# Optimization experiments

Hardware: AMD Instinct MI355X
Metric: run time of the kernel (lower is better)

The kernel has to match this reference:

```python
import jax, jax.numpy as jnp
import numpy as np

E = 131072          # number of message events
NUM_NODES = 32768   # max distinct dst ids (unique padded to this size)
D_MEM = 256         # memory dim
D_EDGE = 128        # edge feature dim
T_DIM = 64          # time encoding dim
HID = 512           # message MLP hidden
MSG = 256           # message dim (GRU input)
IN_DIM = 2 * D_MEM + D_EDGE + T_DIM  # 704


def setup_inputs() -> dict:
    key = jax.random.key(0)
    ks = jax.random.split(key, 16)
    def lin(k, fan_out, fan_in):
        s = 1.0 / np.sqrt(fan_in)
        return jax.random.uniform(k, (fan_out, fan_in), jnp.float32, -s, s)
    def vec(k, n, fan_in):
        s = 1.0 / np.sqrt(fan_in)
        return jax.random.uniform(k, (n,), jnp.float32, -s, s)
    return {
        "rel_time": jax.random.uniform(ks[0], (E,), jnp.float32, 0.0, 1.0) * 1000.0,
        "src_memories": jax.random.normal(ks[1], (E, D_MEM), jnp.float32),
        "dst_memories": jax.random.normal(ks[2], (E, D_MEM), jnp.float32),
        "edge_features": jax.random.normal(ks[3], (E, D_EDGE), jnp.float32),
        "dst_ids": jax.random.randint(ks[4], (E,), 0, NUM_NODES, jnp.int64),
        # time encoder params: cos(t*w + b)
        "time_w": jax.random.normal(ks[5], (T_DIM,), jnp.float32),
        "time_b": jax.random.normal(ks[6], (T_DIM,), jnp.float32),
        # message MLP params
        "w1": lin(ks[7], HID, IN_DIM), "b1": vec(ks[8], HID, IN_DIM),
        "w2": lin(ks[9], MSG, HID), "b2": vec(ks[10], MSG, HID),
        # GRUCell params (torch layout: [3*hidden, in])
        "gru_w_ih": lin(ks[11], 3 * D_MEM, MSG), "gru_w_hh": lin(ks[12], 3 * D_MEM, D_MEM),
        "gru_b_ih": vec(ks[13], 3 * D_MEM, MSG), "gru_b_hh": vec(ks[14], 3 * D_MEM, D_MEM),
    }


def reference(rel_time, src_memories, dst_memories, edge_features, dst_ids,
              time_w, time_b, w1, b1, w2, b2,
              gru_w_ih, gru_w_hh, gru_b_ih, gru_b_hh):
    # --- time encoding: cos(t*w + b) -> [E, T_DIM]
    t_enc = jnp.cos(rel_time[:, None] * time_w[None, :] + time_b[None, :])
    # --- message encoder: MLP over concat(src_mem, dst_mem, edge_feat, t_enc)
    x = jnp.concatenate([src_memories, dst_memories, edge_features, t_enc], axis=-1)  # [E, IN_DIM]
    h = jax.nn.relu(x @ w1.T + b1)
    msg = h @ w2.T + b2  # [E, MSG]
    # --- dedupe dst ids (torch.unique return_inverse), padded to static size
    unique_ids, index = jnp.unique(dst_ids, return_inverse=True,
                                   size=NUM_NODES, fill_value=NUM_NODES)
    # --- mean aggregation of messages per unique dst node
    sums = jax.ops.segment_sum(msg, index, num_segments=NUM_NODES)
    counts = jax.ops.segment_sum(jnp.ones((E,), msg.dtype), index, num_segments=NUM_NODES)
    agg = sums / jnp.maximum(counts, 1.0)[:, None]  # [NUM_NODES, MSG]
    # --- prev memories: torch mem_idx = unique(inverse) = arange(U) -> first rows
    prev = dst_memories[:NUM_NODES]  # [NUM_NODES, D_MEM]
    # --- GRUCell recurrent memory update (torch gate math)
    gi = agg @ gru_w_ih.T + gru_b_ih   # [NUM_NODES, 3*D_MEM]
    gh = prev @ gru_w_hh.T + gru_b_hh
    gi_r, gi_z, gi_n = jnp.split(gi, 3, axis=-1)
    gh_r, gh_z, gh_n = jnp.split(gh, 3, axis=-1)
    r = jax.nn.sigmoid(gi_r + gh_r)
    z = jax.nn.sigmoid(gi_z + gh_z)
    n = jnp.tanh(gi_n + r * gh_n)
    memories = (1.0 - z) * n + z * prev  # [NUM_NODES, D_MEM]
    return unique_ids, memories
```

## Files before the change

### kernel.cpp

```cpp
#include <hip/hip_runtime.h>
#include <math.h>
#include <stdint.h>

#define E_EDGES 131072
#define NN 32768
#define DMEM 256
#define DEDGE 128
#define TDIM 64
#define HID 512
#define MSGD 256
#define INDIM 704

typedef __bf16 bf16_t;
typedef bf16_t bf16x8 __attribute__((ext_vector_type(8)));
typedef float f32x4 __attribute__((ext_vector_type(4)));

__device__ __forceinline__ unsigned short f2bf(float f) {
  unsigned int u = __float_as_uint(f);
  u += 0x7FFF + ((u >> 16) & 1);
  return (unsigned short)(u >> 16);
}

__device__ __forceinline__ void gl_lds16(const bf16_t* g, bf16_t* l) {
  __builtin_amdgcn_global_load_lds(
      (__attribute__((address_space(1))) void*)(g),
      (__attribute__((address_space(3))) void*)(l), 16, 0, 0);
}

__global__ void cvt_bf16(const float* __restrict__ in, unsigned short* __restrict__ out, int n) {
  int i = blockIdx.x * 256 + threadIdx.x;
  if (i < n) out[i] = f2bf(in[i]);
}

__global__ __launch_bounds__(512) void gemm12_fused(
    const float* __restrict__ src, const float* __restrict__ dmem,
    const float* __restrict__ edge, const float* __restrict__ rel,
    const float* __restrict__ tw, const float* __restrict__ tb,
    const bf16_t* __restrict__ w1b, const float* __restrict__ b1,
    const bf16_t* __restrict__ w2b, const float* __restrict__ b2,
    const int* __restrict__ dstid, float* __restrict__ sums) {
  __shared__ alignas(16) bf16_t smem[74752];
  __shared__ float sTW[64], sTB[64], sRel[128];
  bf16_t* sA  = smem;
  bf16_t* sB  = smem + 128 * 32;
  bf16_t* hL  = smem;
  bf16_t* sB2 = smem + 128 * 520;

  const int bm = blockIdx.x;
  const int t = threadIdx.x;
  const int lane = t & 63;
  const int wave = t >> 6;
  const int wm  = (wave >> 2) * 64;
  const int wn1 = (wave & 3) * 128;
  const int wn2 = (wave & 3) * 64;

  if (t < 64) { sTW[t] = tw[t]; sTB[t] = tb[t]; }
  if (t >= 128 && t < 256) sRel[t - 128] = rel[(size_t)bm * 128 + (t - 128)];

  f32x4 acc[4][8];
#pragma unroll
  for (int i = 0; i < 4; i++)
#pragma unroll
    for (int j = 0; j < 8; j++) acc[i][j] = (f32x4){0.f, 0.f, 0.f, 0.f};

  const int ar = t >> 2;
  const int ac = (t & 3) * 8;
  const size_t arow = (size_t)bm * 128 + ar;
  const bf16_t* gB = w1b + (size_t)(t >> 2) * 704 + (t & 3) * 8;
  bf16_t* lB = sB + (size_t)t * 8;

  const int lrow = lane & 15;
  const int kq = (lane >> 4) * 8;

  for (int k0 = 0; k0 < INDIM; k0 += 32) {
    gl_lds16(gB,                     lB);
    gl_lds16(gB + (size_t)128 * 704, lB + 128 * 32);
    gl_lds16(gB + (size_t)256 * 704, lB + 256 * 32);
    gl_lds16(gB + (size_t)384 * 704, lB + 384 * 32);
    gB += 32;

    bf16x8 av;
    if (k0 < 640) {
      const float* p;
      if (k0 < 256)      p = src  + arow * 256 + k0 + ac;
      else if (k0 < 512) p = dmem + arow * 256 + (k0 - 256) + ac;
      else               p = edge + arow * 128 + (k0 - 512) + ac;
      f32x4 u = *(const f32x4*)p;
      f32x4 v = *(const f32x4*)(p + 4);
      av[0] = (bf16_t)u[0]; av[1] = (bf16_t)u[1]; av[2] = (bf16_t)u[2]; av[3] = (bf16_t)u[3];
      av[4] = (bf16_t)v[0]; av[5] = (bf16_t)v[1]; av[6] = (bf16_t)v[2]; av[7] = (bf16_t)v[3];
    } else {
      float rv = sRel[ar];
      int kk = (k0 - 640) + ac;
#pragma unroll
      for (int j = 0; j < 8; j++)
        av[j] = (bf16_t)cosf(rv * sTW[kk + j] + sTB[kk + j]);
    }
    *(bf16x8*)(sA + ar * 32 + ac) = av;

    __syncthreads();
    bf16x8 af[4], bfr[8];
#pragma unroll
    for (int i = 0; i < 4; i++) af[i] = *(const bf16x8*)(sA + (wm + i * 16 + lrow) * 32 + kq);
#pragma unroll
    for (int i = 0; i < 8; i++) bfr[i] = *(const bf16x8*)(sB + (wn1 + i * 16 + lrow) * 32 + kq);
#pragma unroll
    for (int mi = 0; mi < 4; mi++)
#pragma unroll
      for (int ni = 0; ni < 8; ni++)
        acc[mi][ni] = __builtin_amdgcn_mfma_f32_16x16x32_bf16(af[mi], bfr[ni], acc[mi][ni], 0, 0, 0);
    __syncthreads();
  }

  const int crow = (lane >> 4) * 4;
  const int ccol = lane & 15;
#pragma unroll
  for (int ni = 0; ni < 8; ni++) {
    int col = wn1 + ni * 16 + ccol;
    float bv = b1[col];
#pragma unroll
    for (int mi = 0; mi < 4; mi++) {
#pragma unroll
      for (int r = 0; r < 4; r++) {
        float v = fmaxf(acc[mi][ni][r] + bv, 0.f);
        ((unsigned short*)hL)[(wm + mi * 16 + crow + r) * 520 + col] = f2bf(v);
      }
    }
  }

  f32x4 acc2[4][4];
#pragma unroll
  for (int i = 0; i < 4; i++)
#pragma unroll
    for (int j = 0; j < 4; j++) acc2[i][j] = (f32x4){0.f, 0.f, 0.f, 0.f};

  const bf16_t* gW2 = w2b + (size_t)(t >> 2) * 512 + (t & 3) * 8;
  bf16_t* lB2 = sB2 + (size_t)t * 8;

  for (int k0 = 0; k0 < HID; k0 += 32) {
    gl_lds16(gW2,                     lB2);
    gl_lds16(gW2 + (size_t)128 * 512, lB2 + 128 * 32);
    gW2 += 32;
    __syncthreads();
    bf16x8 af2[4], bf2[4];
#pragma unroll
    for (int i = 0; i < 4; i++)
      af2[i] = *(const bf16x8*)(hL + (wm + i * 16 + lrow) * 520 + k0 + kq);
#pragma unroll
    for (int i = 0; i < 4; i++)
      bf2[i] = *(const bf16x8*)(sB2 + (wn2 + i * 16 + lrow) * 32 + kq);
#pragma unroll
    for (int mi = 0; mi < 4; mi++)
#pragma unroll
      for (int ni = 0; ni < 4; ni++)
        acc2[mi][ni] = __builtin_amdgcn_mfma_f32_16x16x32_bf16(af2[mi], bf2[ni], acc2[mi][ni], 0, 0, 0);
    __syncthreads();
  }

#pragma unroll
  for (int mi = 0; mi < 4; mi++) {
    int id4[4];
#pragma unroll
    for (int r = 0; r < 4; r++)
      id4[r] = dstid[(size_t)bm * 128 + wm + mi * 16 + crow + r];
#pragma unroll
    for (int ni = 0; ni < 4; ni++) {
      int gcol = wn2 + ni * 16 + ccol;
      float bv = b2[gcol];
#pragma unroll
      for (int r = 0; r < 4; r++)
        atomicAdd(&sums[(size_t)id4[r] * 256 + gcol], acc2[mi][ni][r] + bv);
    }
  }
}

template <int ACT, int OMODE, int GRUSEL>
__global__ __launch_bounds__(512) void gemm_bt2(
    const bf16_t* __restrict__ A, const bf16_t* __restrict__ B,
    const float* __restrict__ bias, void* __restrict__ Cout,
    const bf16_t* __restrict__ A2, const float* __restrict__ bias2,
    void* __restrict__ Cout2,
    const int* __restrict__ dstid, float* __restrict__ sums,
    int M, int N, int K) {
  __shared__ alignas(16) bf16_t sA[128 * 32];
  __shared__ alignas(16) bf16_t sB[256 * 32];

  int bm = blockIdx.y, bn = blockIdx.x;
  if (GRUSEL && blockIdx.z == 1) { A = A2; bias = bias2; Cout = Cout2; }

  const int t = threadIdx.x;
  const int lane = t & 63;
  const int wave = t >> 6;
  const int wm = (wave >> 2) * 64;
  const int wn = (wave & 3) * 64;

  f32x4 acc[4][4];
#pragma unroll
  for (int i = 0; i < 4; i++)
#pragma unroll
    for (int j = 0; j < 4; j++) acc[i][j] = (f32x4){0.f, 0.f, 0.f, 0.f};

  const int rA = t >> 2;
  const int cA = (t & 3) * 8;
  const bf16_t* gA = A + ((size_t)bm * 128 + rA) * K + cA;
  const bf16_t* gB = B + ((size_t)bn * 256 + rA) * K + cA;
  const size_t gB2off = (size_t)128 * K;
  bf16_t* lA = sA + (size_t)t * 8;
  bf16_t* lB = sB + (size_t)t * 8;

  const int lrow = lane & 15;
  const int kq = (lane >> 4) * 8;

  for (int k0 = 0; k0 < K; k0 += 32) {
    gl_lds16(gA, lA);
    gl_lds16(gB, lB);
    gl_lds16(gB + gB2off, lB + 4096);
    gA += 32; gB += 32;
    __syncthreads();
    bf16x8 af[4], bfr[4];
#pragma unroll
    for (int i = 0; i < 4; i++) af[i] = *(const bf16x8*)(sA + (wm + i * 16 + lrow) * 32 + kq);
#pragma unroll
    for (int i = 0; i < 4; i++) bfr[i] = *(const bf16x8*)(sB + (wn + i * 16 + lrow) * 32 + kq);
#pragma unroll
    for (int mi = 0; mi < 4; mi++)
#pragma unroll
      for (int ni = 0; ni < 4; ni++)
        acc[mi][ni] = __builtin_amdgcn_mfma_f32_16x16x32_bf16(af[mi], bfr[ni], acc[mi][ni], 0, 0, 0);
    __syncthreads();
  }

  const int crow = (lane >> 4) * 4;
  const int ccol = lane & 15;
  if (OMODE == 2) {
#pragma unroll
    for (int mi = 0; mi < 4; mi++) {
      int id4[4];
#pragma unroll
      for (int r = 0; r < 4; r++)
        id4[r] = dstid[(size_t)bm * 128 + wm + mi * 16 + crow + r];
#pragma unroll
      for (int ni = 0; ni < 4; ni++) {
        int gcol = wn + ni * 16 + ccol;
        float bv = bias[gcol];
#pragma unroll
        for (int r = 0; r < 4; r++)
          atomicAdd(&sums[(size_t)id4[r] * 256 + gcol], acc[mi][ni][r] + bv);
      }
    }
  } else {
#pragma unroll
    for (int ni = 0; ni < 4; ni++) {
      int gcol = bn * 256 + wn + ni * 16 + ccol;
      float bv = bias[gcol];
#pragma unroll
      for (int mi = 0; mi < 4; mi++) {
#pragma unroll
        for (int r = 0; r < 4; r++) {
          size_t grow = (size_t)bm * 128 + wm + mi * 16 + crow + r;
          float v = acc[mi][ni][r] + bv;
          if (ACT) v = fmaxf(v, 0.f);
          ((unsigned short*)Cout)[grow * N + gcol] = f2bf(v);
        }
      }
    }
  }
}

__global__ void mark_k(const int* __restrict__ dst, int* __restrict__ flags,
                       float* __restrict__ counts) {
  int e = blockIdx.x * 256 + threadIdx.x;
  if (e < E_EDGES) {
    int id = dst[e];
    flags[id] = 1;
    atomicAdd(&counts[id], 1.0f);
  }
}

__global__ void fill_k(float* __restrict__ uo, int* __restrict__ slot_id) {
  int j = blockIdx.x * 256 + threadIdx.x;
  if (j < NN) { uo[j] = (float)NN; slot_id[j] = -1; }
}

__global__ void scan_k(const int* __restrict__ flags, int* __restrict__ rank) {
  __shared__ int part[1024];
  int t = threadIdx.x;
  int base = t * 32;
  int s = 0;
  for (int i = 0; i < 32; i++) s += flags[base + i];
  part[t] = s;
  __syncthreads();
  for (int off = 1; off < 1024; off <<= 1) {
    int v = (t >= off) ? part[t - off] : 0;
    __syncthreads();
    part[t] += v;
    __syncthreads();
  }
  int run = (t == 0) ? 0 : part[t - 1];
  for (int i = 0; i < 32; i++) { rank[base + i] = run; run += flags[base + i]; }
}

__global__ void scatter_ids(const int* __restrict__ flags, const int* __restrict__ rank,
                            float* __restrict__ uo, int* __restrict__ slot_id) {
  int id = blockIdx.x * 256 + threadIdx.x;
  if (id < NN && flags[id]) {
    int s = rank[id];
    uo[s] = (float)id;
    slot_id[s] = id;
  }
}

__global__ void agg_pack(const int* __restrict__ slot_id, const float* __restrict__ sums,
                         const float* __restrict__ counts, const float* __restrict__ dmem,
                         unsigned short* __restrict__ aggb, unsigned short* __restrict__ prevb) {
  int j = blockIdx.x, t = threadIdx.x;
  int id = slot_id[j];
  float a = 0.f;
  if (id >= 0) a = sums[(size_t)id * 256 + t] / fmaxf(counts[id], 1.f);
  aggb[(size_t)j * 256 + t] = f2bf(a);
  prevb[(size_t)j * 256 + t] = f2bf(dmem[(size_t)j * 256 + t]);
}

__global__ void gru_gate(const unsigned short* __restrict__ gi,
                         const unsigned short* __restrict__ gh,
                         const float* __restrict__ dmem, float* __restrict__ out) {
  int j = blockIdx.x, t = threadIdx.x;
  size_t b = (size_t)j * 768;
  auto bf = [](unsigned short u) { return __uint_as_float((unsigned int)u << 16); };
  float gir = bf(gi[b + t]), giz = bf(gi[b + 256 + t]), gin = bf(gi[b + 512 + t]);
  float ghr = bf(gh[b + t]), ghz = bf(gh[b + 256 + t]), ghn = bf(gh[b + 512 + t]);
  float r = 1.f / (1.f + expf(-(gir + ghr)));
  float z = 1.f / (1.f + expf(-(giz + ghz)));
  float n = tanhf(gin + r * ghn);
  float prev = dmem[(size_t)j * 256 + t];
  out[(size_t)NN + (size_t)j * 256 + t] = (1.f - z) * n + z * prev;
}

extern "C" void kernel_launch(void* const* d_in, const int* in_sizes, int n_in,
                              void* d_out, int out_size, void* d_ws, size_t ws_size,
                              hipStream_t stream) {
  const float* rel  = (const float*)d_in[0];
  const float* src  = (const float*)d_in[1];
  const float* dmem = (const float*)d_in[2];
  const float* edge = (const float*)d_in[3];
  const int*   dst  = (const int*)d_in[4];
  const float* tw   = (const float*)d_in[5];
  const float* tb   = (const float*)d_in[6];
  const float* w1   = (const float*)d_in[7];
  const float* b1   = (const float*)d_in[8];
  const float* w2   = (const float*)d_in[9];
  const float* b2   = (const float*)d_in[10];
  const float* wih  = (const float*)d_in[11];
  const float* whh  = (const float*)d_in[12];
  const float* bih  = (const float*)d_in[13];
  const float* bhh  = (const float*)d_in[14];

  char* ws = (char*)d_ws;
  size_t o = 0;
  auto take = [&](size_t bytes) -> char* {
    char* p = ws + o;
    o += (bytes + 255) & ~(size_t)255;
    return p;
  };

  unsigned short* gib   = (unsigned short*)take((size_t)NN * 768 * 2);
  unsigned short* ghb   = (unsigned short*)take((size_t)NN * 768 * 2);
  float* sums           = (float*)take((size_t)NN * 256 * 4);
  float* counts         = (float*)take((size_t)NN * 4);
  int*   flags          = (int*)take((size_t)NN * 4);
  int*   rank           = (int*)take((size_t)NN * 4);
  int*   slot_id        = (int*)take((size_t)NN * 4);
  unsigned short* aggb  = (unsigned short*)take((size_t)NN * 256 * 2);
  unsigned short* prevb = (unsigned short*)take((size_t)NN * 256 * 2);
  unsigned short* w1b   = (unsigned short*)take((size_t)HID * INDIM * 2);
  unsigned short* w2b   = (unsigned short*)take((size_t)MSGD * HID * 2);
  unsigned short* wihb  = (unsigned short*)take((size_t)768 * 256 * 2);
  unsigned short* whhb  = (unsigned short*)take((size_t)768 * 256 * 2);

  float* outf = (float*)d_out;

  hipMemsetAsync(sums, 0, (size_t)NN * 256 * 4, stream);
  hipMemsetAsync(counts, 0, (size_t)NN * 4, stream);
  hipMemsetAsync(flags, 0, (size_t)NN * 4, stream);

  int n1 = HID * INDIM;
  int n2 = MSGD * HID;
  int n3 = 768 * 256;
  cvt_bf16<<<(n1 + 255) / 256, 256, 0, stream>>>(w1, w1b, n1);
  cvt_bf16<<<(n2 + 255) / 256, 256, 0, stream>>>(w2, w2b, n2);
  cvt_bf16<<<(n3 + 255) / 256, 256, 0, stream>>>(wih, wihb, n3);
  cvt_bf16<<<(n3 + 255) / 256, 256, 0, stream>>>(whh, whhb, n3);

  mark_k<<<E_EDGES / 256, 256, 0, stream>>>(dst, flags, counts);

  gemm12_fused<<<dim3(E_EDGES / 128), 512, 0, stream>>>(
      src, dmem, edge, rel, tw, tb, (const bf16_t*)w1b, b1,
      (const bf16_t*)w2b, b2, dst, sums);

  fill_k<<<NN / 256, 256, 0, stream>>>(outf, slot_id);
  scan_k<<<1, 1024, 0, stream>>>(flags, rank);
  scatter_ids<<<NN / 256, 256, 0, stream>>>(flags, rank, outf, slot_id);
  agg_pack<<<NN, 256, 0, stream>>>(slot_id, sums, counts, dmem, aggb, prevb);

  gemm_bt2<0, 1, 1><<<dim3(768 / 256, NN / 128, 2), 512, 0, stream>>>(
      (const bf16_t*)aggb, (const bf16_t*)wihb, bih, gib,
      (const bf16_t*)prevb, bhh, ghb, nullptr, nullptr, NN, 768, 256);

  gru_gate<<<NN, 256, 0, stream>>>(gib, ghb, dmem, outf);
}
```

Before: 723.2 us.

## Sort edges by destination and reduce messages in LDS before scatter

Builds a counting-sort permutation of edges by dst id (histogram, scan for offsets, atomic cursor scatter). The fused MLP kernel then loads rows through this permutation, so each 128-row tile holds runs of equal destinations. Each run is summed in shared memory and written once, with atomics only for runs touching tile boundaries. This replaces 128×256 global float atomics per tile with mostly plain stores, at the cost of gathered row loads, an extra sort pass and a barrier.

```diff
diff --git a/kernel.cpp b/kernel.cpp
--- a/kernel.cpp
+++ b/kernel.cpp
@@ -38,9 +38,11 @@
     const float* __restrict__ tw, const float* __restrict__ tb,
     const bf16_t* __restrict__ w1b, const float* __restrict__ b1,
     const bf16_t* __restrict__ w2b, const float* __restrict__ b2,
-    const int* __restrict__ dstid, float* __restrict__ sums) {
+    const int* __restrict__ perm, const int* __restrict__ dsts,
+    float* __restrict__ sums) {
   __shared__ alignas(16) bf16_t smem[74752];
   __shared__ float sTW[64], sTB[64], sRel[128];
+  __shared__ int sPerm[128], sDst[128];
   bf16_t* sA  = smem;
   bf16_t* sB  = smem + 128 * 32;
   bf16_t* hL  = smem;
@@ -55,7 +57,13 @@
   const int wn2 = (wave & 3) * 64;
 
   if (t < 64) { sTW[t] = tw[t]; sTB[t] = tb[t]; }
-  if (t >= 128 && t < 256) sRel[t - 128] = rel[(size_t)bm * 128 + (t - 128)];
+  if (t < 128) {
+    int e = perm[bm * 128 + t];
+    sPerm[t] = e;
+    sRel[t] = rel[e];
+    sDst[t] = dsts[bm * 128 + t];
+  }
+  __syncthreads();
 
   f32x4 acc[4][8];
 #pragma unroll
@@ -65,7 +73,7 @@
 
   const int ar = t >> 2;
   const int ac = (t & 3) * 8;
-  const size_t arow = (size_t)bm * 128 + ar;
+  const size_t arow = (size_t)sPerm[ar];
   const bf16_t* gB = w1b + (size_t)(t >> 2) * 704 + (t & 3) * 8;
   bf16_t* lB = sB + (size_t)t * 8;
 
@@ -157,19 +165,36 @@
     __syncthreads();
   }
 
-#pragma unroll
-  for (int mi = 0; mi < 4; mi++) {
-    int id4[4];
-#pragma unroll
-    for (int r = 0; r < 4; r++)
-      id4[r] = dstid[(size_t)bm * 128 + wm + mi * 16 + crow + r];
+  {
+    float* msgL = (float*)smem;
 #pragma unroll
     for (int ni = 0; ni < 4; ni++) {
       int gcol = wn2 + ni * 16 + ccol;
       float bv = b2[gcol];
 #pragma unroll
-      for (int r = 0; r < 4; r++)
-        atomicAdd(&sums[(size_t)id4[r] * 256 + gcol], acc2[mi][ni][r] + bv);
+      for (int mi = 0; mi < 4; mi++) {
+#pragma unroll
+        for (int r = 0; r < 4; r++)
+          msgL[(wm + mi * 16 + crow + r) * 260 + gcol] = acc2[mi][ni][r] + bv;
+      }
+    }
+    __syncthreads();
+
+    const int c = t & 255;
+    const int h = t >> 8;
+    int r = h * 64;
+    const int rend = h * 64 + 64;
+    while (r < rend) {
+      int id = sDst[r];
+      if (r > 0 && sDst[r - 1] == id) { r++; continue; }
+      float s2 = msgL[r * 260 + c];
+      int rr = r + 1;
+      while (rr < 128 && sDst[rr] == id) { s2 += msgL[rr * 260 + c]; rr++; }
+      if (r == 0 || rr == 128)
+        atomicAdd(&sums[(size_t)id * 256 + c], s2);
+      else
+        sums[(size_t)id * 256 + c] = s2;
+      r = rr;
     }
   }
 }
@@ -267,56 +292,70 @@
   }
 }
 
-__global__ void mark_k(const int* __restrict__ dst, int* __restrict__ flags,
-                       float* __restrict__ counts) {
+__global__ void mark_k(const int* __restrict__ dst, int* __restrict__ icnt) {
+  int e = blockIdx.x * 256 + threadIdx.x;
+  if (e < E_EDGES) atomicAdd(&icnt[dst[e]], 1);
+}
+
+__global__ void fill_k(float* __restrict__ uo, int* __restrict__ slot_id) {
+  int j = blockIdx.x * 256 + threadIdx.x;
+  if (j < NN) { uo[j] = (float)NN; slot_id[j] = -1; }
+}
+
+__global__ void scan2_k(const int* __restrict__ icnt, int* __restrict__ rank,
+                        int* __restrict__ offs) {
+  __shared__ int pf[1024], pc[1024];
+  int t = threadIdx.x;
+  int base = t * 32;
+  int sf = 0, sc = 0;
+  for (int i = 0; i < 32; i++) { int v = icnt[base + i]; sf += (v > 0); sc += v; }
+  pf[t] = sf; pc[t] = sc;
+  __syncthreads();
+  for (int off = 1; off < 1024; off <<= 1) {
+    int vf = (t >= off) ? pf[t - off] : 0;
+    int vc = (t >= off) ? pc[t - off] : 0;
+    __syncthreads();
+    pf[t] += vf; pc[t] += vc;
+    __syncthreads();
+  }
+  int runf = (t == 0) ? 0 : pf[t - 1];
+  int runc = (t == 0) ? 0 : pc[t - 1];
+  for (int i = 0; i < 32; i++) {
+    int v = icnt[base + i];
+    rank[base + i] = runf; runf += (v > 0);
+    offs[base + i] = runc; runc += v;
+  }
+}
+
+__global__ void scatter_ids(const int* __restrict__ icnt, const int* __restrict__ rank,
+                            float* __restrict__ uo, int* __restrict__ slot_id) {
+  int id = blockIdx.x * 256 + threadIdx.x;
+  if (id < NN && icnt[id] > 0) {
+    int s = rank[id];
+    uo[s] = (float)id;
+    slot_id[s] = id;
+  }
+}
+
+__global__ void scatter_edges(const int* __restrict__ dst, const int* __restrict__ offs,
+                              int* __restrict__ cursor, int* __restrict__ perm,
+                              int* __restrict__ dsts) {
   int e = blockIdx.x * 256 + threadIdx.x;
   if (e < E_EDGES) {
     int id = dst[e];
-    flags[id] = 1;
-    atomicAdd(&counts[id], 1.0f);
-  }
-}
-
-__global__ void fill_k(float* __restrict__ uo, int* __restrict__ slot_id) {
-  int j = blockIdx.x * 256 + threadIdx.x;
-  if (j < NN) { uo[j] = (float)NN; slot_id[j] = -1; }
-}
-
-__global__ void scan_k(const int* __restrict__ flags, int* __restrict__ rank) {
-  __shared__ int part[1024];
-  int t = threadIdx.x;
-  int base = t * 32;
-  int s = 0;
-  for (int i = 0; i < 32; i++) s += flags[base + i];
-  part[t] = s;
-  __syncthreads();
-  for (int off = 1; off < 1024; off <<= 1) {
-    int v = (t >= off) ? part[t - off] : 0;
-    __syncthreads();
-    part[t] += v;
-    __syncthreads();
-  }
-  int run = (t == 0) ? 0 : part[t - 1];
-  for (int i = 0; i < 32; i++) { rank[base + i] = run; run += flags[base + i]; }
-}
-
-__global__ void scatter_ids(const int* __restrict__ flags, const int* __restrict__ rank,
-                            float* __restrict__ uo, int* __restrict__ slot_id) {
-  int id = blockIdx.x * 256 + threadIdx.x;
-  if (id < NN && flags[id]) {
-    int s = rank[id];
-    uo[s] = (float)id;
-    slot_id[s] = id;
+    int pos = offs[id] + atomicAdd(&cursor[id], 1);
+    perm[pos] = e;
+    dsts[pos] = id;
   }
 }
 
 __global__ void agg_pack(const int* __restrict__ slot_id, const float* __restrict__ sums,
-                         const float* __restrict__ counts, const float* __restrict__ dmem,
+                         const int* __restrict__ icnt, const float* __restrict__ dmem,
                          unsigned short* __restrict__ aggb, unsigned short* __restrict__ prevb) {
   int j = blockIdx.x, t = threadIdx.x;
   int id = slot_id[j];
   float a = 0.f;
-  if (id >= 0) a = sums[(size_t)id * 256 + t] / fmaxf(counts[id], 1.f);
+  if (id >= 0) a = sums[(size_t)id * 256 + t] / fmaxf((float)icnt[id], 1.f);
   aggb[(size_t)j * 256 + t] = f2bf(a);
   prevb[(size_t)j * 256 + t] = f2bf(dmem[(size_t)j * 256 + t]);
 }
@@ -366,10 +405,13 @@
   unsigned short* gib   = (unsigned short*)take((size_t)NN * 768 * 2);
   unsigned short* ghb   = (unsigned short*)take((size_t)NN * 768 * 2);
   float* sums           = (float*)take((size_t)NN * 256 * 4);
-  float* counts         = (float*)take((size_t)NN * 4);
-  int*   flags          = (int*)take((size_t)NN * 4);
+  int*   icnt           = (int*)take((size_t)NN * 4);
   int*   rank           = (int*)take((size_t)NN * 4);
+  int*   offs           = (int*)take((size_t)NN * 4);
+  int*   cursor         = (int*)take((size_t)NN * 4);
   int*   slot_id        = (int*)take((size_t)NN * 4);
+  int*   perm           = (int*)take((size_t)E_EDGES * 4);
+  int*   dsts           = (int*)take((size_t)E_EDGES * 4);
   unsigned short* aggb  = (unsigned short*)take((size_t)NN * 256 * 2);
   unsigned short* prevb = (unsigned short*)take((size_t)NN * 256 * 2);
   unsigned short* w1b   = (unsigned short*)take((size_t)HID * INDIM * 2);
@@ -380,8 +422,8 @@
   float* outf = (float*)d_out;
 
   hipMemsetAsync(sums, 0, (size_t)NN * 256 * 4, stream);
-  hipMemsetAsync(counts, 0, (size_t)NN * 4, stream);
-  hipMemsetAsync(flags, 0, (size_t)NN * 4, stream);
+  hipMemsetAsync(icnt, 0, (size_t)NN * 4, stream);
+  hipMemsetAsync(cursor, 0, (size_t)NN * 4, stream);
 
   int n1 = HID * INDIM;
   int n2 = MSGD * HID;
@@ -391,16 +433,18 @@
   cvt_bf16<<<(n3 + 255) / 256, 256, 0, stream>>>(wih, wihb, n3);
   cvt_bf16<<<(n3 + 255) / 256, 256, 0, stream>>>(whh, whhb, n3);
 
-  mark_k<<<E_EDGES / 256, 256, 0, stream>>>(dst, flags, counts);
+  mark_k<<<E_EDGES / 256, 256, 0, stream>>>(dst, icnt);
+  scan2_k<<<1, 1024, 0, stream>>>(icnt, rank, offs);
+  scatter_edges<<<E_EDGES / 256, 256, 0, stream>>>(dst, offs, cursor, perm, dsts);
+
+  fill_k<<<NN / 256, 256, 0, stream>>>(outf, slot_id);
+  scatter_ids<<<NN / 256, 256, 0, stream>>>(icnt, rank, outf, slot_id);
 
   gemm12_fused<<<dim3(E_EDGES / 128), 512, 0, stream>>>(
       src, dmem, edge, rel, tw, tb, (const bf16_t*)w1b, b1,
-      (const bf16_t*)w2b, b2, dst, sums);
-
-  fill_k<<<NN / 256, 256, 0, stream>>>(outf, slot_id);
-  scan_k<<<1, 1024, 0, stream>>>(flags, rank);
-  scatter_ids<<<NN / 256, 256, 0, stream>>>(flags, rank, outf, slot_id);
-  agg_pack<<<NN, 256, 0, stream>>>(slot_id, sums, counts, dmem, aggb, prevb);
+      (const bf16_t*)w2b, b2, perm, dsts, sums);
+
+  agg_pack<<<NN, 256, 0, stream>>>(slot_id, sums, icnt, dmem, aggb, prevb);
 
   gemm_bt2<0, 1, 1><<<dim3(768 / 256, NN / 128, 2), 512, 0, stream>>>(
       (const bf16_t*)aggb, (const bf16_t*)wihb, bih, gib,
```

Result: faster. 703.2 us (-2.8%).
